# Kernel optimization log

Measured on AMD Instinct MI355X. Metric: run time of the kernel, lower is better.

Reference implementation:

```python
import jax, jax.numpy as jnp
import numpy as np

B, C, H, W = 32, 128, 64, 64
K = 512  # num_embeddings


def setup_inputs() -> dict:
    key = jax.random.key(0)
    k1, k2 = jax.random.split(key)
    z_e = jax.random.normal(k1, (B, C, H, W), dtype=jnp.float32)
    # nn.Embedding init: uniform(-1/K, 1/K)
    embedding = jax.random.uniform(k2, (K, C), dtype=jnp.float32,
                                   minval=-1.0 / K, maxval=1.0 / K)
    return {"z_e": z_e, "embedding": embedding}


def reference(z_e, embedding):
    b, c, h, w = z_e.shape
    # permute(0,2,3,1).reshape(-1, C)
    z_flat = jnp.transpose(z_e, (0, 2, 3, 1)).reshape(-1, c)  # [N, C]
    # Faithful to source: distances lack the -2 z.e cross term (repo bug).
    distances = (jnp.sum(z_flat * z_flat, axis=1, keepdims=True)
                 + jnp.sum(embedding * embedding, axis=1))  # [N, K]
    indices = jnp.argmin(distances, axis=1)  # [N]
    z_q = embedding[indices].reshape(b, h, w, c)  # gather + view
    z_q = jnp.transpose(z_q, (0, 3, 1, 2))  # [B, C, H, W]
    codebook_loss = jnp.mean(jnp.square(z_q - jax.lax.stop_gradient(z_e)))
    commitment_loss = jnp.mean(jnp.square(jax.lax.stop_gradient(z_q) - z_e))
    vq_loss = codebook_loss + commitment_loss
    return z_q, vq_loss
```

## Files before the change

kernel.cpp:

```cpp
#include <hip/hip_runtime.h>


#define NZ   16777216
#define NZ4  4194304
#define KEMB 512
#define CEMB 128

__global__ __launch_bounds__(512) void vq_prep(const float* __restrict__ emb,
                                               float* __restrict__ ws_eq,
                                               float* __restrict__ loss_ptr) {
    __shared__ float s_norm[KEMB];
    __shared__ int   s_best;

    const int t = threadIdx.x;
    const float4* e4 = (const float4*)emb;
    float acc = 0.f;
    #pragma unroll
    for (int i = 0; i < CEMB / 4; ++i) {
        float4 v = e4[t * (CEMB / 4) + i];
        acc += v.x * v.x + v.y * v.y + v.z * v.z + v.w * v.w;
    }
    s_norm[t] = acc;
    __syncthreads();

    if (t < 64) {
        float bv = s_norm[t * 8];
        int   bi = t * 8;
        #pragma unroll
        for (int j = 1; j < 8; ++j) {
            float v = s_norm[t * 8 + j];
            if (v < bv) { bv = v; bi = t * 8 + j; }
        }
        #pragma unroll
        for (int off = 32; off > 0; off >>= 1) {
            float ov = __shfl_down(bv, off);
            int   oi = __shfl_down(bi, off);
            if (ov < bv || (ov == bv && oi < bi)) { bv = ov; bi = oi; }
        }
        if (t == 0) {
            s_best = bi;
            loss_ptr[0] = 0.f;
        }
    }
    __syncthreads();
    if (t < CEMB) ws_eq[t] = emb[s_best * CEMB + t];
}

__global__ __launch_bounds__(256) void vq_main(const float4* __restrict__ ze4,
                                               float4* __restrict__ zq4,
                                               const float* __restrict__ eq,
                                               float* __restrict__ loss_ptr) {
    float lsum = 0.f;
    const int stride = gridDim.x * blockDim.x;
    for (int i = blockIdx.x * blockDim.x + threadIdx.x; i < NZ4; i += stride) {
        float4 z = ze4[i];
        int c = (i >> 10) & (CEMB - 1);
        float e = eq[c];
        float4 q = make_float4(e, e, e, e);
        zq4[i] = q;
        float d0 = e - z.x, d1 = e - z.y, d2 = e - z.z, d3 = e - z.w;
        lsum += d0 * d0 + d1 * d1 + d2 * d2 + d3 * d3;
    }
    #pragma unroll
    for (int off = 32; off > 0; off >>= 1) lsum += __shfl_down(lsum, off);
    __shared__ float s_w[4];
    const int lane = threadIdx.x & 63, wid = threadIdx.x >> 6;
    if (lane == 0) s_w[wid] = lsum;
    __syncthreads();
    if (threadIdx.x == 0) {
        float s = s_w[0] + s_w[1] + s_w[2] + s_w[3];
        atomicAdd(loss_ptr, s * (2.0f / (float)NZ));
    }
}

extern "C" void kernel_launch(void* const* d_in, const int* in_sizes, int n_in,
                              void* d_out, int out_size, void* d_ws, size_t ws_size,
                              hipStream_t stream) {
    const float* z_e = (const float*)d_in[0];
    const float* emb = (const float*)d_in[1];
    float* out      = (float*)d_out;
    float* zq       = out;
    float* loss_ptr = out + NZ;
    float* ws_eq    = (float*)d_ws;

    vq_prep<<<1, 512, 0, stream>>>(emb, ws_eq, loss_ptr);
    vq_main<<<2048, 256, 0, stream>>>((const float4*)z_e, (float4*)zq, ws_eq, loss_ptr);
}
```

Measured before the change: 139.9 us.

## Parallelize codebook norm argmin and unroll streaming main kernel with nontemporal access

The single-block norm/argmin prep kernel is replaced by a 128-block kernel. Each wavefront computes one embedding row's norm and publishes it through a 64-bit packed atomicMin, after a memset initialises the slot. The main kernel drops its grid-stride loop: each thread issues eight independent nontemporal 16-byte loads and stores and gathers the selected embedding value directly. This aims to cut the serial prep latency and raise memory-level parallelism in the bandwidth-bound pass, at the cost of an extra memset launch and a global atomic.

```diff
diff --git a/kernel.cpp b/kernel.cpp
--- a/kernel.cpp
+++ b/kernel.cpp
@@ -3,64 +3,75 @@
 
 #define NZ   16777216
 #define NZ4  4194304
+#define NTHR 524288
 #define KEMB 512
 #define CEMB 128
 
-__global__ __launch_bounds__(512) void vq_prep(const float* __restrict__ emb,
-                                               float* __restrict__ ws_eq,
-                                               float* __restrict__ loss_ptr) {
-    __shared__ float s_norm[KEMB];
-    __shared__ int   s_best;
+typedef float f32x4 __attribute__((ext_vector_type(4)));
 
-    const int t = threadIdx.x;
-    const float4* e4 = (const float4*)emb;
-    float acc = 0.f;
+__global__ __launch_bounds__(256) void vq_norms(const float* __restrict__ emb,
+                                                unsigned long long* __restrict__ ws_min,
+                                                float* __restrict__ loss_ptr) {
+    const int lane = threadIdx.x & 63;
+    const int wid  = threadIdx.x >> 6;
+    const int row  = blockIdx.x * 4 + wid;
+
+    const float2 v = ((const float2*)emb)[row * 64 + lane];
+    float n = v.x * v.x + v.y * v.y;
     #pragma unroll
-    for (int i = 0; i < CEMB / 4; ++i) {
-        float4 v = e4[t * (CEMB / 4) + i];
-        acc += v.x * v.x + v.y * v.y + v.z * v.z + v.w * v.w;
+    for (int off = 32; off > 0; off >>= 1) n += __shfl_down(n, off);
+
+    if (lane == 0) {
+        unsigned long long packed =
+            ((unsigned long long)__float_as_uint(n) << 32) | (unsigned int)row;
+        atomicMin(ws_min, packed);
     }
-    s_norm[t] = acc;
-    __syncthreads();
-
-    if (t < 64) {
-        float bv = s_norm[t * 8];
-        int   bi = t * 8;
-        #pragma unroll
-        for (int j = 1; j < 8; ++j) {
-            float v = s_norm[t * 8 + j];
-            if (v < bv) { bv = v; bi = t * 8 + j; }
-        }
-        #pragma unroll
-        for (int off = 32; off > 0; off >>= 1) {
-            float ov = __shfl_down(bv, off);
-            int   oi = __shfl_down(bi, off);
-            if (ov < bv || (ov == bv && oi < bi)) { bv = ov; bi = oi; }
-        }
-        if (t == 0) {
-            s_best = bi;
-            loss_ptr[0] = 0.f;
-        }
-    }
-    __syncthreads();
-    if (t < CEMB) ws_eq[t] = emb[s_best * CEMB + t];
+    if (blockIdx.x == 0 && threadIdx.x == 0) loss_ptr[0] = 0.f;
 }
 
-__global__ __launch_bounds__(256) void vq_main(const float4* __restrict__ ze4,
-                                               float4* __restrict__ zq4,
-                                               const float* __restrict__ eq,
+__global__ __launch_bounds__(256) void vq_main(const f32x4* __restrict__ ze4,
+                                               f32x4* __restrict__ zq4,
+                                               const float* __restrict__ emb,
+                                               const unsigned long long* __restrict__ ws_min,
                                                float* __restrict__ loss_ptr) {
+    const int tid = blockIdx.x * 256 + threadIdx.x;
+
+    const int c = (tid >> 10) & (CEMB - 1);
+    const int best = (int)(unsigned int)(*ws_min & 0xffffffffull);
+    const float e = emb[best * CEMB + c];
+
+    f32x4 z0 = __builtin_nontemporal_load(ze4 + tid + 0 * NTHR);
+    f32x4 z1 = __builtin_nontemporal_load(ze4 + tid + 1 * NTHR);
+    f32x4 z2 = __builtin_nontemporal_load(ze4 + tid + 2 * NTHR);
+    f32x4 z3 = __builtin_nontemporal_load(ze4 + tid + 3 * NTHR);
+    f32x4 z4 = __builtin_nontemporal_load(ze4 + tid + 4 * NTHR);
+    f32x4 z5 = __builtin_nontemporal_load(ze4 + tid + 5 * NTHR);
+    f32x4 z6 = __builtin_nontemporal_load(ze4 + tid + 6 * NTHR);
+    f32x4 z7 = __builtin_nontemporal_load(ze4 + tid + 7 * NTHR);
+
+    const f32x4 q = {e, e, e, e};
+    __builtin_nontemporal_store(q, zq4 + tid + 0 * NTHR);
+    __builtin_nontemporal_store(q, zq4 + tid + 1 * NTHR);
+    __builtin_nontemporal_store(q, zq4 + tid + 2 * NTHR);
+    __builtin_nontemporal_store(q, zq4 + tid + 3 * NTHR);
+    __builtin_nontemporal_store(q, zq4 + tid + 4 * NTHR);
+    __builtin_nontemporal_store(q, zq4 + tid + 5 * NTHR);
+    __builtin_nontemporal_store(q, zq4 + tid + 6 * NTHR);
+    __builtin_nontemporal_store(q, zq4 + tid + 7 * NTHR);
+
     float lsum = 0.f;
-    const int stride = gridDim.x * blockDim.x;
-    for (int i = blockIdx.x * blockDim.x + threadIdx.x; i < NZ4; i += stride) {
-        float4 z = ze4[i];
-        int c = (i >> 10) & (CEMB - 1);
-        float e = eq[c];
-        float4 q = make_float4(e, e, e, e);
-        zq4[i] = q;
-        float d0 = e - z.x, d1 = e - z.y, d2 = e - z.z, d3 = e - z.w;
-        lsum += d0 * d0 + d1 * d1 + d2 * d2 + d3 * d3;
+    {
+        f32x4 d;
+        d = z0 - q; lsum += d.x*d.x + d.y*d.y + d.z*d.z + d.w*d.w;
+        d = z1 - q; lsum += d.x*d.x + d.y*d.y + d.z*d.z + d.w*d.w;
+        d = z2 - q; lsum += d.x*d.x + d.y*d.y + d.z*d.z + d.w*d.w;
+        d = z3 - q; lsum += d.x*d.x + d.y*d.y + d.z*d.z + d.w*d.w;
+        d = z4 - q; lsum += d.x*d.x + d.y*d.y + d.z*d.z + d.w*d.w;
+        d = z5 - q; lsum += d.x*d.x + d.y*d.y + d.z*d.z + d.w*d.w;
+        d = z6 - q; lsum += d.x*d.x + d.y*d.y + d.z*d.z + d.w*d.w;
+        d = z7 - q; lsum += d.x*d.x + d.y*d.y + d.z*d.z + d.w*d.w;
     }
+
     #pragma unroll
     for (int off = 32; off > 0; off >>= 1) lsum += __shfl_down(lsum, off);
     __shared__ float s_w[4];
@@ -78,11 +89,11 @@
                               hipStream_t stream) {
     const float* z_e = (const float*)d_in[0];
     const float* emb = (const float*)d_in[1];
-    float* out      = (float*)d_out;
-    float* zq       = out;
-    float* loss_ptr = out + NZ;
-    float* ws_eq    = (float*)d_ws;
+    float* out       = (float*)d_out;
+    float* loss_ptr  = out + NZ;
+    unsigned long long* ws_min = (unsigned long long*)d_ws;
 
-    vq_prep<<<1, 512, 0, stream>>>(emb, ws_eq, loss_ptr);
-    vq_main<<<2048, 256, 0, stream>>>((const float4*)z_e, (float4*)zq, ws_eq, loss_ptr);
+    hipMemsetAsync(d_ws, 0xFF, 8, stream);
+    vq_norms<<<KEMB / 4 / 64 * 64, 256, 0, stream>>>(emb, ws_min, loss_ptr);
+    vq_main<<<2048, 256, 0, stream>>>((const f32x4*)z_e, (f32x4*)out, emb, ws_min, loss_ptr);
 }
```

Measured after the change: 137.1 us. 2.0% less time.
